# Performance work log

Measured on AMD Instinct MI355X. Metric: run time of the kernel, lower is better.

The kernel has to match this reference:

```python
import jax, jax.numpy as jnp
import numpy as np

B, S, V, E, D, C = 128, 256, 50000, 300, 200, 3

def setup_inputs() -> dict:
    key = jax.random.key(0)
    ks = jax.random.split(key, 16)
    std = 0.01  # truncated_normal(stddev=0.01) in the original
    d = {
        'x1': jax.random.randint(ks[0], (B, S), 0, V, dtype=jnp.int32),
        'x2': jax.random.randint(ks[1], (B, S), 0, V, dtype=jnp.int32),
        'len1': jax.random.randint(ks[2], (B,), 1, S + 1, dtype=jnp.int32),
        'len2': jax.random.randint(ks[3], (B,), 1, S + 1, dtype=jnp.int32),
        'emb': jax.random.normal(ks[4], (V, E), jnp.float32),
        'W_proj': jax.random.normal(ks[5], (E, D), jnp.float32) * std,
        'F_W1': jax.random.normal(ks[6], (D, D), jnp.float32) * std,
        'F_b1': jnp.zeros((D,), jnp.float32),
        'F_W2': jax.random.normal(ks[7], (D, D), jnp.float32) * std,
        'F_b2': jnp.zeros((D,), jnp.float32),
        'G_W1': jax.random.normal(ks[8], (2 * D, D), jnp.float32) * std,
        'G_b1': jnp.zeros((D,), jnp.float32),
        'G_W2': jax.random.normal(ks[9], (D, D), jnp.float32) * std,
        'G_b2': jnp.zeros((D,), jnp.float32),
        'H_W1': jax.random.normal(ks[10], (2 * D, D), jnp.float32) * std,
        'H_b1': jnp.zeros((D,), jnp.float32),
        'H_W2': jax.random.normal(ks[11], (D, D), jnp.float32) * std,
        'H_b2': jnp.zeros((D,), jnp.float32),
        'W_out': jax.random.normal(ks[12], (D, C), jnp.float32) * std,
        'b_out': jnp.zeros((C,), jnp.float32),
    }
    return d


def _mlp(x, W1, b1, W2, b2):
    # two dense layers, relu after each (activation_fn defaults to relu)
    h = jax.nn.relu(x @ W1 + b1)
    return jax.nn.relu(h @ W2 + b2)


def reference(x1, x2, len1, len2, emb, W_proj,
              F_W1, F_b1, F_W2, F_b2,
              G_W1, G_b1, G_W2, G_b2,
              H_W1, H_b1, H_W2, H_b2,
              W_out, b_out):
    seq = x1.shape[1]
    # masks: [B, S, 1]
    pos = jnp.arange(seq)
    mask1 = (pos[None, :] < len1[:, None]).astype(jnp.float32)[..., None]
    mask2 = (pos[None, :] < len2[:, None]).astype(jnp.float32)[..., None]

    # embed (L2-normalized table) + project to D
    emb_n = emb * jax.lax.rsqrt(jnp.sum(emb * emb, axis=1, keepdims=True))
    e1, e2 = emb_n[x1], emb_n[x2]          # [B,S,E]
    x1p, x2p = e1 @ W_proj, e2 @ W_proj    # [B,S,D]

    # attend: F(x1) . F(x2) -> [B,S1,S2] (broadcast-mul-reduce == contraction)
    f1 = _mlp(x1p, F_W1, F_b1, F_W2, F_b2)
    f2 = _mlp(x2p, F_W1, F_b1, F_W2, F_b2)
    sim = jnp.einsum('bid,bjd->bij', f1, f2)
    sim = sim * (mask1 * jnp.swapaxes(mask2, 1, 2))  # multiplicative mask (as in source)

    alpha = jnp.einsum('bji,bid->bjd', jax.nn.softmax(jnp.swapaxes(sim, 1, 2), axis=-1), x1p)  # [B,S2,D]
    beta = jnp.einsum('bij,bjd->bid', jax.nn.softmax(sim, axis=-1), x2p)                        # [B,S1,D]

    # compare
    v1 = _mlp(jnp.concatenate([x1p, beta], axis=2), G_W1, G_b1, G_W2, G_b2)
    v2 = _mlp(jnp.concatenate([x2p, alpha], axis=2), G_W1, G_b1, G_W2, G_b2)

    # aggregate
    v1 = jnp.sum(v1 * mask1, axis=1)  # [B,D]
    v2 = jnp.sum(v2 * mask2, axis=1)
    h = _mlp(jnp.concatenate([v1, v2], axis=1), H_W1, H_b1, H_W2, H_b2)
    y_hat = h @ W_out + b_out  # [B,C] logits
    return y_hat
```

## Files before the change

kernel.cpp:

```cpp
#include <hip/hip_runtime.h>
#include <math.h>

#define B_ 128
#define S_ 256
#define V_ 50000
#define E_ 300
#define D_ 200
#define C_ 3
#define P_ 256
#define TOK_ (B_*S_)

typedef __attribute__((ext_vector_type(8))) short bf16x8;
typedef __attribute__((ext_vector_type(4))) float f32x4;

static __device__ __forceinline__ short f2bf(float f) {
  unsigned u = __builtin_bit_cast(unsigned, f);
  u += 0x7fffu + ((u >> 16) & 1u);
  return (short)(u >> 16);
}
static __device__ __forceinline__ float bf2f(unsigned short u) {
  unsigned v = ((unsigned)u) << 16;
  return __builtin_bit_cast(float, v);
}

__global__ void pad2d_kernel(const float* __restrict__ src, float* __restrict__ dst,
                             int sR, int sC, int dR, int dC) {
  int idx = blockIdx.x * 256 + threadIdx.x;
  if (idx >= dR * dC) return;
  int r = idx / dC, c = idx - r * dC;
  dst[idx] = (r < sR && c < sC) ? src[r * sC + c] : 0.0f;
}

__global__ void padcat_kernel(const float* __restrict__ src, float* __restrict__ dst) {
  int idx = blockIdx.x * 256 + threadIdx.x;
  if (idx >= 512 * 256) return;
  int r = idx >> 8, c = idx & 255;
  int sr = (r < 200) ? r : ((r >= 256 && r < 456) ? (r - 56) : -1);
  dst[idx] = (sr >= 0 && c < 200) ? src[sr * 200 + c] : 0.0f;
}

__global__ void padT_bf16(const float* __restrict__ src, unsigned short* __restrict__ dst,
                          int sK, int sN, int dK, int dN) {
  int idx = blockIdx.x * 256 + threadIdx.x;
  if (idx >= dN * dK) return;
  int n = idx / dK, k = idx - n * dK;
  float v = (k < sK && n < sN) ? src[k * sN + n] : 0.0f;
  dst[idx] = (unsigned short)f2bf(v);
}

__global__ void padcatT_bf16(const float* __restrict__ src, unsigned short* __restrict__ dst) {
  int idx = blockIdx.x * 256 + threadIdx.x;
  if (idx >= 256 * 512) return;
  int n = idx >> 9, k = idx & 511;
  int sk = (k < 256) ? ((k < 200) ? k : -1) : (((k - 256) < 200) ? (200 + k - 256) : -1);
  float v = (sk >= 0 && n < 200) ? src[sk * 200 + n] : 0.0f;
  dst[idx] = (unsigned short)f2bf(v);
}

__global__ void zero_kernel(float* __restrict__ p, int n) {
  int idx = blockIdx.x * 256 + threadIdx.x;
  if (idx < n) p[idx] = 0.0f;
}

__global__ void concat_ids_kernel(const int* __restrict__ a, const int* __restrict__ b,
                                  int* __restrict__ dst) {
  int i = blockIdx.x * 256 + threadIdx.x;
  if (i < TOK_) dst[i] = a[i];
  else if (i < 2 * TOK_) dst[i] = b[i - TOK_];
}

__global__ void concat_lens_kernel(const int* __restrict__ a, const int* __restrict__ b,
                                   int* __restrict__ dst) {
  int i = threadIdx.x;
  if (i < B_) dst[i] = a[i];
  else dst[i] = b[i - B_];
}

__global__ __launch_bounds__(256) void invnorm_kernel(const int* __restrict__ ids,
    const float* __restrict__ emb, float* __restrict__ invn) {
  int tok = blockIdx.x * 4 + (threadIdx.x >> 6);
  int l = threadIdx.x & 63;
  long base = (long)ids[tok] * E_;
  float ss = 0.0f;
  for (int e = l; e < E_; e += 64) { float v = emb[base + e]; ss += v * v; }
  #pragma unroll
  for (int d = 32; d >= 1; d >>= 1) ss += __shfl_xor(ss, d, 64);
  if (l == 0) invn[tok] = 1.0f / sqrtf(ss);
}

__global__ __launch_bounds__(256) void transpose_bf16(
    const unsigned short* __restrict__ in, unsigned short* __restrict__ outp) {
  __shared__ unsigned short t[64][66];
  const int b = blockIdx.x;
  const int r0 = blockIdx.y * 64, c0 = blockIdx.z * 64;
  const unsigned short* src = in + (long)b * S_ * P_;
  unsigned short* dst = outp + (long)b * P_ * S_;
  const int tx = threadIdx.x & 63, ty = threadIdx.x >> 6;
  #pragma unroll
  for (int i = 0; i < 16; ++i)
    t[ty * 16 + i][tx] = src[(long)(r0 + ty * 16 + i) * P_ + c0 + tx];
  __syncthreads();
  #pragma unroll
  for (int i = 0; i < 16; ++i)
    dst[(long)(c0 + ty * 16 + i) * S_ + r0 + tx] = t[tx][ty * 16 + i];
}

template<int MODE, bool RELU, bool AGG>
__global__ __launch_bounds__(512) void gemm_mfma(
    const unsigned short* __restrict__ A1, const unsigned short* __restrict__ A2,
    const int* __restrict__ ids, const float* __restrict__ emb,
    const float* __restrict__ invn,
    const unsigned short* __restrict__ WT, const float* __restrict__ bias,
    unsigned short* __restrict__ outp, float* __restrict__ aggOut,
    const int* __restrict__ lens, int K)
{
  __shared__ unsigned short As[128 * 32];
  __shared__ unsigned short Bs[256 * 32];
  const int tid = threadIdx.x;
  const int lane = tid & 63;
  const int w = tid >> 6;
  const int wr = w >> 2, wc = w & 3;
  const long t0 = (long)blockIdx.x * 128;
  const int g = lane >> 4, ln = lane & 15;

  f32x4 acc[4][4];
  #pragma unroll
  for (int i = 0; i < 4; ++i)
    #pragma unroll
    for (int j = 0; j < 4; ++j) acc[i][j] = (f32x4){0.f, 0.f, 0.f, 0.f};

  const int arow = tid >> 2, aks = tid & 3;

  for (int k0 = 0; k0 < K; k0 += 32) {
    {
      bf16x8 v;
      if (MODE == 1) {
        const long t = t0 + arow;
        const long base = (long)ids[t] * E_;
        const float inv = invn[t];
        const int kb = k0 + aks * 8;
        short tmp[8];
        #pragma unroll
        for (int i = 0; i < 8; ++i) {
          const int k = kb + i;
          tmp[i] = f2bf((k < E_) ? emb[base + k] * inv : 0.0f);
        }
        #pragma unroll
        for (int i = 0; i < 8; ++i) v[i] = tmp[i];
      } else if (MODE == 2) {
        const unsigned short* src = (k0 < P_) ? (A1 + (t0 + arow) * P_ + k0)
                                              : (A2 + (t0 + arow) * P_ + (k0 - P_));
        v = *(const bf16x8*)(src + aks * 8);
      } else {
        v = *(const bf16x8*)(A1 + (t0 + arow) * P_ + k0 + aks * 8);
      }
      const int slot = aks ^ ((arow >> 1) & 3);
      *(bf16x8*)&As[arow * 32 + slot * 8] = v;
    }
    #pragma unroll
    for (int cc = 0; cc < 2; ++cc) {
      const int c = tid + cc * 512;
      const int col = c >> 2, ks = c & 3;
      bf16x8 v = *(const bf16x8*)(WT + (long)col * K + k0 + ks * 8);
      const int slot = ks ^ ((col >> 1) & 3);
      *(bf16x8*)&Bs[col * 32 + slot * 8] = v;
    }
    __syncthreads();
    bf16x8 af[4], bfr[4];
    #pragma unroll
    for (int fr = 0; fr < 4; ++fr) {
      const int row = wr * 64 + fr * 16 + ln;
      af[fr] = *(const bf16x8*)&As[row * 32 + ((g ^ ((row >> 1) & 3)) * 8)];
    }
    #pragma unroll
    for (int fc = 0; fc < 4; ++fc) {
      const int col = wc * 64 + fc * 16 + ln;
      bfr[fc] = *(const bf16x8*)&Bs[col * 32 + ((g ^ ((col >> 1) & 3)) * 8)];
    }
    #pragma unroll
    for (int fr = 0; fr < 4; ++fr)
      #pragma unroll
      for (int fc = 0; fc < 4; ++fc)
        acc[fr][fc] = __builtin_amdgcn_mfma_f32_16x16x32_bf16(af[fr], bfr[fc], acc[fr][fc], 0, 0, 0);
    __syncthreads();
  }

  const int g4 = g * 4;
  if (AGG) {
    const int b = (int)(t0 >> 8);
    const int s0 = (int)(t0 & 255);
    const int len = lens[b];
    #pragma unroll
    for (int fc = 0; fc < 4; ++fc) {
      const int col = wc * 64 + fc * 16 + ln;
      const float bb = bias[col];
      float sum = 0.0f;
      #pragma unroll
      for (int fr = 0; fr < 4; ++fr) {
        const int sbase = s0 + wr * 64 + fr * 16 + g4;
        #pragma unroll
        for (int r = 0; r < 4; ++r) {
          if (sbase + r < len) sum += fmaxf(acc[fr][fc][r] + bb, 0.0f);
        }
      }
      sum += __shfl_xor(sum, 16, 64);
      sum += __shfl_xor(sum, 32, 64);
      if (g == 0) atomicAdd(&aggOut[(long)b * P_ + col], sum);
    }
  } else {
    #pragma unroll
    for (int fc = 0; fc < 4; ++fc) {
      const int col = wc * 64 + fc * 16 + ln;
      const float bb = bias ? bias[col] : 0.0f;
      #pragma unroll
      for (int fr = 0; fr < 4; ++fr) {
        const long rbase = t0 + wr * 64 + fr * 16 + g4;
        #pragma unroll
        for (int r = 0; r < 4; ++r) {
          float v = acc[fr][fc][r] + bb;
          if (RELU) v = fmaxf(v, 0.0f);
          outp[(rbase + r) * P_ + col] = (unsigned short)f2bf(v);
        }
      }
    }
  }
}

__global__ __launch_bounds__(512) void attend_fused(
    const unsigned short* __restrict__ f12, const unsigned short* __restrict__ x12T,
    const int* __restrict__ lens12, unsigned short* __restrict__ out12)
{
  __shared__ unsigned short As[128 * 32];
  __shared__ unsigned short Bs[256 * 32];
  __shared__ unsigned short Pt[128 * 256];
  __shared__ float redmax[128][4];
  __shared__ float redsum[128][4];

  const int tid = threadIdx.x;
  const int lane = tid & 63;
  const int w = tid >> 6;
  const int wr = w >> 2, wc = w & 3;
  const int b = blockIdx.y;
  const int z = blockIdx.z;
  const int i0 = blockIdx.x * 128;
  const int g = lane >> 4, ln = lane & 15;

  const unsigned short* Afeat = f12 + (size_t)z * TOK_ * P_;
  const unsigned short* Bfeat = f12 + (size_t)(1 - z) * TOK_ * P_;
  const unsigned short* XT    = x12T + (size_t)(1 - z) * TOK_ * P_;
  unsigned short* outp        = out12 + (size_t)z * TOK_ * P_;
  const int l1 = lens12[z * B_ + b];
  const int l2 = lens12[(1 - z) * B_ + b];

  const unsigned short* Arows = Afeat + ((long)b * S_ + i0) * P_;
  const unsigned short* Brows = Bfeat + (long)b * S_ * P_;

  f32x4 acc[4][4];
  #pragma unroll
  for (int i = 0; i < 4; ++i)
    #pragma unroll
    for (int j = 0; j < 4; ++j) acc[i][j] = (f32x4){0.f, 0.f, 0.f, 0.f};

  const int arow = tid >> 2, aks = tid & 3;
  for (int k0 = 0; k0 < P_; k0 += 32) {
    {
      bf16x8 v = *(const bf16x8*)(Arows + (long)arow * P_ + k0 + aks * 8);
      const int slot = aks ^ ((arow >> 1) & 3);
      *(bf16x8*)&As[arow * 32 + slot * 8] = v;
    }
    #pragma unroll
    for (int cc = 0; cc < 2; ++cc) {
      const int c = tid + cc * 512;
      const int col = c >> 2, ks = c & 3;
      bf16x8 v = *(const bf16x8*)(Brows + (long)col * P_ + k0 + ks * 8);
      const int slot = ks ^ ((col >> 1) & 3);
      *(bf16x8*)&Bs[col * 32 + slot * 8] = v;
    }
    __syncthreads();
    bf16x8 af[4], bfr[4];
    #pragma unroll
    for (int fr = 0; fr < 4; ++fr) {
      const int row = wr * 64 + fr * 16 + ln;
      af[fr] = *(const bf16x8*)&As[row * 32 + ((g ^ ((row >> 1) & 3)) * 8)];
    }
    #pragma unroll
    for (int fc = 0; fc < 4; ++fc) {
      const int col = wc * 64 + fc * 16 + ln;
      bfr[fc] = *(const bf16x8*)&Bs[col * 32 + ((g ^ ((col >> 1) & 3)) * 8)];
    }
    #pragma unroll
    for (int fr = 0; fr < 4; ++fr)
      #pragma unroll
      for (int fc = 0; fc < 4; ++fc)
        acc[fr][fc] = __builtin_amdgcn_mfma_f32_16x16x32_bf16(af[fr], bfr[fc], acc[fr][fc], 0, 0, 0);
    __syncthreads();
  }

  const int g4 = g * 4;
  #pragma unroll
  for (int fr = 0; fr < 4; ++fr) {
    #pragma unroll
    for (int fc = 0; fc < 4; ++fc) {
      const int col = wc * 64 + fc * 16 + ln;
      const float mj = (col < l2) ? 1.0f : 0.0f;
      #pragma unroll
      for (int r = 0; r < 4; ++r) {
        const int rowg = i0 + wr * 64 + fr * 16 + g4 + r;
        acc[fr][fc][r] *= (rowg < l1) ? mj : 0.0f;
      }
    }
  }
  #pragma unroll
  for (int fr = 0; fr < 4; ++fr) {
    #pragma unroll
    for (int r = 0; r < 4; ++r) {
      float m = fmaxf(fmaxf(acc[fr][0][r], acc[fr][1][r]),
                      fmaxf(acc[fr][2][r], acc[fr][3][r]));
      m = fmaxf(m, __shfl_xor(m, 1, 64));
      m = fmaxf(m, __shfl_xor(m, 2, 64));
      m = fmaxf(m, __shfl_xor(m, 4, 64));
      m = fmaxf(m, __shfl_xor(m, 8, 64));
      if (ln == 0) redmax[wr * 64 + fr * 16 + g4 + r][wc] = m;
    }
  }
  __syncthreads();
  #pragma unroll
  for (int fr = 0; fr < 4; ++fr) {
    #pragma unroll
    for (int r = 0; r < 4; ++r) {
      const int lr = wr * 64 + fr * 16 + g4 + r;
      const float4 m4 = *(const float4*)redmax[lr];
      const float m = fmaxf(fmaxf(m4.x, m4.y), fmaxf(m4.z, m4.w));
      float s = 0.0f;
      #pragma unroll
      for (int fc = 0; fc < 4; ++fc) {
        const float e = __expf(acc[fr][fc][r] - m);
        acc[fr][fc][r] = e;
        s += e;
      }
      s += __shfl_xor(s, 1, 64);
      s += __shfl_xor(s, 2, 64);
      s += __shfl_xor(s, 4, 64);
      s += __shfl_xor(s, 8, 64);
      if (ln == 0) redsum[lr][wc] = s;
    }
  }
  __syncthreads();
  #pragma unroll
  for (int fr = 0; fr < 4; ++fr) {
    #pragma unroll
    for (int r = 0; r < 4; ++r) {
      const int lr = wr * 64 + fr * 16 + g4 + r;
      const float4 s4 = *(const float4*)redsum[lr];
      const float inv = 1.0f / (s4.x + s4.y + s4.z + s4.w);
      #pragma unroll
      for (int fc = 0; fc < 4; ++fc) {
        const int col = wc * 64 + fc * 16 + ln;
        Pt[lr * 256 + ((col & ~31) | ((((col >> 3) & 3) ^ ((lr >> 1) & 3)) << 3) | (col & 7))] =
            (unsigned short)f2bf(acc[fr][fc][r] * inv);
      }
    }
  }

  f32x4 acc2[4][4];
  #pragma unroll
  for (int i = 0; i < 4; ++i)
    #pragma unroll
    for (int j = 0; j < 4; ++j) acc2[i][j] = (f32x4){0.f, 0.f, 0.f, 0.f};
  const unsigned short* XTb = XT + (long)b * P_ * S_;
  for (int k0 = 0; k0 < S_; k0 += 32) {
    #pragma unroll
    for (int cc = 0; cc < 2; ++cc) {
      const int c = tid + cc * 512;
      const int col = c >> 2, ks = c & 3;
      bf16x8 v = *(const bf16x8*)(XTb + (long)col * S_ + k0 + ks * 8);
      const int slot = ks ^ ((col >> 1) & 3);
      *(bf16x8*)&Bs[col * 32 + slot * 8] = v;
    }
    __syncthreads();
    bf16x8 af[4], bfr[4];
    #pragma unroll
    for (int fr = 0; fr < 4; ++fr) {
      const int row = wr * 64 + fr * 16 + ln;
      af[fr] = *(const bf16x8*)&Pt[row * 256 + k0 + ((g ^ ((row >> 1) & 3)) * 8)];
    }
    #pragma unroll
    for (int fc = 0; fc < 4; ++fc) {
      const int col = wc * 64 + fc * 16 + ln;
      bfr[fc] = *(const bf16x8*)&Bs[col * 32 + ((g ^ ((col >> 1) & 3)) * 8)];
    }
    #pragma unroll
    for (int fr = 0; fr < 4; ++fr)
      #pragma unroll
      for (int fc = 0; fc < 4; ++fc)
        acc2[fr][fc] = __builtin_amdgcn_mfma_f32_16x16x32_bf16(af[fr], bfr[fc], acc2[fr][fc], 0, 0, 0);
    __syncthreads();
  }

  #pragma unroll
  for (int fc = 0; fc < 4; ++fc) {
    const int col = wc * 64 + fc * 16 + ln;
    #pragma unroll
    for (int fr = 0; fr < 4; ++fr) {
      const long rbase = (long)b * S_ + i0 + wr * 64 + fr * 16 + g4;
      #pragma unroll
      for (int r = 0; r < 4; ++r)
        outp[(rbase + r) * P_ + col] = (unsigned short)f2bf(acc2[fr][fc][r]);
    }
  }
}

__global__ __launch_bounds__(256) void head_kernel(
    const float* __restrict__ v1s, const float* __restrict__ v2s,
    const float* __restrict__ HW1p, const float* __restrict__ Hb1p,
    const float* __restrict__ HW2p, const float* __restrict__ Hb2p,
    const float* __restrict__ Wout, const float* __restrict__ bout,
    float* __restrict__ y)
{
  __shared__ float xin[2 * P_];
  __shared__ float h[P_];
  const int b = blockIdx.x;
  const int tid = threadIdx.x;
  xin[tid] = v1s[(long)b * P_ + tid];
  xin[P_ + tid] = v2s[(long)b * P_ + tid];
  __syncthreads();
  float acc = Hb1p[tid];
  for (int e = 0; e < 2 * P_; ++e) acc += xin[e] * HW1p[(long)e * P_ + tid];
  h[tid] = fmaxf(acc, 0.0f);
  __syncthreads();
  float acc2 = Hb2p[tid];
  for (int e = 0; e < P_; ++e) acc2 += h[e] * HW2p[(long)e * P_ + tid];
  const float h2 = fmaxf(acc2, 0.0f);
  __syncthreads();
  xin[tid] = h2;
  __syncthreads();
  if (tid < C_) {
    float a = bout[tid];
    for (int d = 0; d < D_; ++d) a += xin[d] * Wout[d * C_ + tid];
    y[(long)b * C_ + tid] = a;
  }
}

extern "C" void kernel_launch(void* const* d_in, const int* in_sizes, int n_in,
                              void* d_out, int out_size, void* d_ws, size_t ws_size,
                              hipStream_t stream)
{
  const int*   x1    = (const int*)d_in[0];
  const int*   x2    = (const int*)d_in[1];
  const int*   len1  = (const int*)d_in[2];
  const int*   len2  = (const int*)d_in[3];
  const float* emb   = (const float*)d_in[4];
  const float* Wproj = (const float*)d_in[5];
  const float* FW1   = (const float*)d_in[6];
  const float* Fb1   = (const float*)d_in[7];
  const float* FW2   = (const float*)d_in[8];
  const float* Fb2   = (const float*)d_in[9];
  const float* GW1   = (const float*)d_in[10];
  const float* Gb1   = (const float*)d_in[11];
  const float* GW2   = (const float*)d_in[12];
  const float* Gb2   = (const float*)d_in[13];
  const float* HW1   = (const float*)d_in[14];
  const float* Hb1   = (const float*)d_in[15];
  const float* HW2   = (const float*)d_in[16];
  const float* Hb2   = (const float*)d_in[17];
  const float* Wout  = (const float*)d_in[18];
  const float* bout  = (const float*)d_in[19];
  float* out = (float*)d_out;

  float* ws = (float*)d_ws;
  size_t o = 0;
  auto alloc = [&](size_t n) { float* p = ws + o; o += n; return p; };
  float* v12   = alloc((size_t)2 * B_ * P_);
  float* invn12 = alloc((size_t)2 * TOK_);
  float* HW1p  = alloc((size_t)2 * P_ * P_); float* Hb1p = alloc(P_);
  float* HW2p  = alloc((size_t)P_ * P_);     float* Hb2p = alloc(P_);
  float* Fb1p  = alloc(P_); float* Fb2p = alloc(P_);
  float* Gb1p  = alloc(P_); float* Gb2p = alloc(P_);
  int* ids12  = (int*)alloc((size_t)2 * TOK_);
  int* lens12 = (int*)alloc(2 * B_);
  unsigned short* us = (unsigned short*)(ws + o);
  size_t uo = 0;
  auto ualloc = [&](size_t n) { unsigned short* p = us + uo; uo += n; return p; };
  unsigned short* x12b  = ualloc((size_t)2 * TOK_ * P_);
  unsigned short* hid2b = ualloc((size_t)2 * TOK_ * P_);
  unsigned short* f12b  = ualloc((size_t)2 * TOK_ * P_);
  unsigned short* ba12b = ualloc((size_t)2 * TOK_ * P_);
  unsigned short* x12T  = ualloc((size_t)2 * TOK_ * P_);
  unsigned short* WpT   = ualloc((size_t)P_ * 320);
  unsigned short* FW1T  = ualloc((size_t)P_ * P_);
  unsigned short* FW2T  = ualloc((size_t)P_ * P_);
  unsigned short* GW1T  = ualloc((size_t)P_ * 2 * P_);
  unsigned short* GW2T  = ualloc((size_t)P_ * P_);
  if (o * sizeof(float) + uo * sizeof(unsigned short) > ws_size) return;

  float* v1s = v12;
  float* v2s = v12 + (size_t)B_ * P_;

  auto g = [](int n) { return (n + 255) / 256; };

  padT_bf16<<<g(P_ * 320), 256, 0, stream>>>(Wproj, WpT, E_, D_, 320, P_);
  padT_bf16<<<g(P_ * P_), 256, 0, stream>>>(FW1, FW1T, D_, D_, P_, P_);
  padT_bf16<<<g(P_ * P_), 256, 0, stream>>>(FW2, FW2T, D_, D_, P_, P_);
  padT_bf16<<<g(P_ * P_), 256, 0, stream>>>(GW2, GW2T, D_, D_, P_, P_);
  padcatT_bf16<<<g(P_ * 2 * P_), 256, 0, stream>>>(GW1, GW1T);
  padcat_kernel<<<g(2 * P_ * P_), 256, 0, stream>>>(HW1, HW1p);
  pad2d_kernel<<<g(P_ * P_), 256, 0, stream>>>(HW2, HW2p, D_, D_, P_, P_);
  pad2d_kernel<<<1, 256, 0, stream>>>(Fb1, Fb1p, 1, D_, 1, P_);
  pad2d_kernel<<<1, 256, 0, stream>>>(Fb2, Fb2p, 1, D_, 1, P_);
  pad2d_kernel<<<1, 256, 0, stream>>>(Gb1, Gb1p, 1, D_, 1, P_);
  pad2d_kernel<<<1, 256, 0, stream>>>(Gb2, Gb2p, 1, D_, 1, P_);
  pad2d_kernel<<<1, 256, 0, stream>>>(Hb1, Hb1p, 1, D_, 1, P_);
  pad2d_kernel<<<1, 256, 0, stream>>>(Hb2, Hb2p, 1, D_, 1, P_);
  zero_kernel<<<g(2 * B_ * P_), 256, 0, stream>>>(v12, 2 * B_ * P_);
  concat_ids_kernel<<<g(2 * TOK_), 256, 0, stream>>>(x1, x2, ids12);
  concat_lens_kernel<<<1, 256, 0, stream>>>(len1, len2, lens12);

  invnorm_kernel<<<2 * TOK_ / 4, 256, 0, stream>>>(ids12, emb, invn12);
  gemm_mfma<1, false, false><<<2 * TOK_ / 128, 512, 0, stream>>>(
      nullptr, nullptr, ids12, emb, invn12, WpT, nullptr, x12b, nullptr, nullptr, 320);

  {
    dim3 grid(2 * B_, 4, 4);
    transpose_bf16<<<grid, 256, 0, stream>>>(x12b, x12T);
  }

  gemm_mfma<0, true, false><<<2 * TOK_ / 128, 512, 0, stream>>>(
      x12b, nullptr, nullptr, nullptr, nullptr, FW1T, Fb1p, hid2b, nullptr, nullptr, P_);
  gemm_mfma<0, true, false><<<2 * TOK_ / 128, 512, 0, stream>>>(
      hid2b, nullptr, nullptr, nullptr, nullptr, FW2T, Fb2p, f12b, nullptr, nullptr, P_);

  {
    dim3 grid(S_ / 128, B_, 2);
    attend_fused<<<grid, 512, 0, stream>>>(f12b, x12T, lens12, ba12b);
  }

  gemm_mfma<2, true, false><<<2 * TOK_ / 128, 512, 0, stream>>>(
      x12b, ba12b, nullptr, nullptr, nullptr, GW1T, Gb1p, hid2b, nullptr, nullptr, 2 * P_);
  gemm_mfma<0, true, true><<<2 * TOK_ / 128, 512, 0, stream>>>(
      hid2b, nullptr, nullptr, nullptr, nullptr, GW2T, Gb2p, nullptr, v12, lens12, P_);

  head_kernel<<<B_, 256, 0, stream>>>(v1s, v2s, HW1p, Hb1p, HW2p, Hb2p, Wout, bout, out);
}
```

Baseline: 411.7 us.

## Fuse MLP layer pairs, merge prep kernels, widen blocks to 1024 threads

Merges the sixteen small padding, transpose, zero and concat kernels into one prep_all launch. Fuses each two-layer MLP (F and G) into one kernel that keeps the hidden activation in LDS, so the bf16 intermediate never goes to global memory. The fused MLP and attend kernels now use 1024 threads with 16 waves, each wave holding a 64x32 tile. The cost is 64KB+ of LDS per block and 16 waves per workgroup, which lowers occupancy and adds sync overhead.

```diff
diff --git a/kernel.cpp b/kernel.cpp
--- a/kernel.cpp
+++ b/kernel.cpp
@@ -18,62 +18,69 @@
   u += 0x7fffu + ((u >> 16) & 1u);
   return (short)(u >> 16);
 }
-static __device__ __forceinline__ float bf2f(unsigned short u) {
-  unsigned v = ((unsigned)u) << 16;
-  return __builtin_bit_cast(float, v);
-}
-
-__global__ void pad2d_kernel(const float* __restrict__ src, float* __restrict__ dst,
-                             int sR, int sC, int dR, int dC) {
-  int idx = blockIdx.x * 256 + threadIdx.x;
-  if (idx >= dR * dC) return;
-  int r = idx / dC, c = idx - r * dC;
-  dst[idx] = (r < sR && c < sC) ? src[r * sC + c] : 0.0f;
-}
-
-__global__ void padcat_kernel(const float* __restrict__ src, float* __restrict__ dst) {
-  int idx = blockIdx.x * 256 + threadIdx.x;
-  if (idx >= 512 * 256) return;
-  int r = idx >> 8, c = idx & 255;
-  int sr = (r < 200) ? r : ((r >= 256 && r < 456) ? (r - 56) : -1);
-  dst[idx] = (sr >= 0 && c < 200) ? src[sr * 200 + c] : 0.0f;
-}
-
-__global__ void padT_bf16(const float* __restrict__ src, unsigned short* __restrict__ dst,
-                          int sK, int sN, int dK, int dN) {
-  int idx = blockIdx.x * 256 + threadIdx.x;
-  if (idx >= dN * dK) return;
-  int n = idx / dK, k = idx - n * dK;
-  float v = (k < sK && n < sN) ? src[k * sN + n] : 0.0f;
-  dst[idx] = (unsigned short)f2bf(v);
-}
-
-__global__ void padcatT_bf16(const float* __restrict__ src, unsigned short* __restrict__ dst) {
-  int idx = blockIdx.x * 256 + threadIdx.x;
-  if (idx >= 256 * 512) return;
-  int n = idx >> 9, k = idx & 511;
-  int sk = (k < 256) ? ((k < 200) ? k : -1) : (((k - 256) < 200) ? (200 + k - 256) : -1);
-  float v = (sk >= 0 && n < 200) ? src[sk * 200 + n] : 0.0f;
-  dst[idx] = (unsigned short)f2bf(v);
-}
-
-__global__ void zero_kernel(float* __restrict__ p, int n) {
-  int idx = blockIdx.x * 256 + threadIdx.x;
-  if (idx < n) p[idx] = 0.0f;
-}
-
-__global__ void concat_ids_kernel(const int* __restrict__ a, const int* __restrict__ b,
-                                  int* __restrict__ dst) {
-  int i = blockIdx.x * 256 + threadIdx.x;
-  if (i < TOK_) dst[i] = a[i];
-  else if (i < 2 * TOK_) dst[i] = b[i - TOK_];
-}
-
-__global__ void concat_lens_kernel(const int* __restrict__ a, const int* __restrict__ b,
-                                   int* __restrict__ dst) {
-  int i = threadIdx.x;
-  if (i < B_) dst[i] = a[i];
-  else dst[i] = b[i - B_];
+
+__global__ __launch_bounds__(256) void prep_all(
+    const float* __restrict__ Wproj, const float* __restrict__ FW1,
+    const float* __restrict__ FW2, const float* __restrict__ GW1,
+    const float* __restrict__ GW2, const float* __restrict__ HW1,
+    const float* __restrict__ HW2,
+    const float* __restrict__ Fb1, const float* __restrict__ Fb2,
+    const float* __restrict__ Gb1, const float* __restrict__ Gb2,
+    const float* __restrict__ Hb1, const float* __restrict__ Hb2,
+    const int* __restrict__ x1, const int* __restrict__ x2,
+    const int* __restrict__ len1, const int* __restrict__ len2,
+    unsigned short* __restrict__ WpT, unsigned short* __restrict__ FW1T,
+    unsigned short* __restrict__ FW2T, unsigned short* __restrict__ GW1T,
+    unsigned short* __restrict__ GW2T, float* __restrict__ HW1p,
+    float* __restrict__ HW2p, float* __restrict__ biases,
+    float* __restrict__ v12, int* __restrict__ ids12, int* __restrict__ lens12)
+{
+  const int blk = blockIdx.x;
+  const int tid = threadIdx.x;
+  if (blk < 320) {
+    int idx = blk * 256 + tid;
+    int n = idx / 320, k = idx - n * 320;
+    WpT[idx] = (unsigned short)f2bf((k < E_ && n < D_) ? Wproj[k * D_ + n] : 0.0f);
+  } else if (blk < 576) {
+    int idx = (blk - 320) * 256 + tid;
+    int n = idx >> 8, k = idx & 255;
+    FW1T[idx] = (unsigned short)f2bf((k < D_ && n < D_) ? FW1[k * D_ + n] : 0.0f);
+  } else if (blk < 832) {
+    int idx = (blk - 576) * 256 + tid;
+    int n = idx >> 8, k = idx & 255;
+    FW2T[idx] = (unsigned short)f2bf((k < D_ && n < D_) ? FW2[k * D_ + n] : 0.0f);
+  } else if (blk < 1088) {
+    int idx = (blk - 832) * 256 + tid;
+    int n = idx >> 8, k = idx & 255;
+    GW2T[idx] = (unsigned short)f2bf((k < D_ && n < D_) ? GW2[k * D_ + n] : 0.0f);
+  } else if (blk < 1600) {
+    int idx = (blk - 1088) * 256 + tid;
+    int n = idx >> 9, k = idx & 511;
+    int sk = (k < 256) ? ((k < D_) ? k : -1) : (((k - 256) < D_) ? (D_ + k - 256) : -1);
+    GW1T[idx] = (unsigned short)f2bf((sk >= 0 && n < D_) ? GW1[sk * D_ + n] : 0.0f);
+  } else if (blk < 2112) {
+    int idx = (blk - 1600) * 256 + tid;
+    int r = idx >> 8, c = idx & 255;
+    int sr = (r < D_) ? r : ((r >= 256 && r < 256 + D_) ? (r - 56) : -1);
+    HW1p[idx] = (sr >= 0 && c < D_) ? HW1[sr * D_ + c] : 0.0f;
+  } else if (blk < 2368) {
+    int idx = (blk - 2112) * 256 + tid;
+    int r = idx >> 8, c = idx & 255;
+    HW2p[idx] = (r < D_ && c < D_) ? HW2[r * D_ + c] : 0.0f;
+  } else if (blk < 2374) {
+    int j = blk - 2368;
+    const float* src = (j == 0) ? Fb1 : (j == 1) ? Fb2 : (j == 2) ? Gb1
+                      : (j == 3) ? Gb2 : (j == 4) ? Hb1 : Hb2;
+    biases[j * 256 + tid] = (tid < D_) ? src[tid] : 0.0f;
+  } else if (blk < 2630) {
+    v12[(blk - 2374) * 256 + tid] = 0.0f;
+  } else if (blk < 2886) {
+    int idx = (blk - 2630) * 256 + tid;
+    ids12[idx] = (idx < TOK_) ? x1[idx] : x2[idx - TOK_];
+  } else {
+    if (tid < B_) lens12[tid] = len1[tid];
+    else if (tid < 2 * B_) lens12[tid] = len2[tid - B_];
+  }
 }
 
 __global__ __launch_bounds__(256) void invnorm_kernel(const int* __restrict__ ids,
@@ -105,14 +112,10 @@
     dst[(long)(c0 + ty * 16 + i) * S_ + r0 + tx] = t[tx][ty * 16 + i];
 }
 
-template<int MODE, bool RELU, bool AGG>
-__global__ __launch_bounds__(512) void gemm_mfma(
-    const unsigned short* __restrict__ A1, const unsigned short* __restrict__ A2,
+__global__ __launch_bounds__(512) void proj_mfma(
     const int* __restrict__ ids, const float* __restrict__ emb,
-    const float* __restrict__ invn,
-    const unsigned short* __restrict__ WT, const float* __restrict__ bias,
-    unsigned short* __restrict__ outp, float* __restrict__ aggOut,
-    const int* __restrict__ lens, int K)
+    const float* __restrict__ invn, const unsigned short* __restrict__ WT,
+    unsigned short* __restrict__ outp, int K)
 {
   __shared__ unsigned short As[128 * 32];
   __shared__ unsigned short Bs[256 * 32];
@@ -130,30 +133,21 @@
     for (int j = 0; j < 4; ++j) acc[i][j] = (f32x4){0.f, 0.f, 0.f, 0.f};
 
   const int arow = tid >> 2, aks = tid & 3;
-
   for (int k0 = 0; k0 < K; k0 += 32) {
     {
+      const long t = t0 + arow;
+      const long base = (long)ids[t] * E_;
+      const float inv = invn[t];
+      const int kb = k0 + aks * 8;
+      short tmp[8];
+      #pragma unroll
+      for (int i = 0; i < 8; ++i) {
+        const int k = kb + i;
+        tmp[i] = f2bf((k < E_) ? emb[base + k] * inv : 0.0f);
+      }
       bf16x8 v;
-      if (MODE == 1) {
-        const long t = t0 + arow;
-        const long base = (long)ids[t] * E_;
-        const float inv = invn[t];
-        const int kb = k0 + aks * 8;
-        short tmp[8];
-        #pragma unroll
-        for (int i = 0; i < 8; ++i) {
-          const int k = kb + i;
-          tmp[i] = f2bf((k < E_) ? emb[base + k] * inv : 0.0f);
-        }
-        #pragma unroll
-        for (int i = 0; i < 8; ++i) v[i] = tmp[i];
-      } else if (MODE == 2) {
-        const unsigned short* src = (k0 < P_) ? (A1 + (t0 + arow) * P_ + k0)
-                                              : (A2 + (t0 + arow) * P_ + (k0 - P_));
-        v = *(const bf16x8*)(src + aks * 8);
-      } else {
-        v = *(const bf16x8*)(A1 + (t0 + arow) * P_ + k0 + aks * 8);
-      }
+      #pragma unroll
+      for (int i = 0; i < 8; ++i) v[i] = tmp[i];
       const int slot = aks ^ ((arow >> 1) & 3);
       *(bf16x8*)&As[arow * 32 + slot * 8] = v;
     }
@@ -184,23 +178,149 @@
         acc[fr][fc] = __builtin_amdgcn_mfma_f32_16x16x32_bf16(af[fr], bfr[fc], acc[fr][fc], 0, 0, 0);
     __syncthreads();
   }
-
   const int g4 = g * 4;
+  #pragma unroll
+  for (int fc = 0; fc < 4; ++fc) {
+    const int col = wc * 64 + fc * 16 + ln;
+    #pragma unroll
+    for (int fr = 0; fr < 4; ++fr) {
+      const long rbase = t0 + wr * 64 + fr * 16 + g4;
+      #pragma unroll
+      for (int r = 0; r < 4; ++r)
+        outp[(rbase + r) * P_ + col] = (unsigned short)f2bf(acc[fr][fc][r]);
+    }
+  }
+}
+
+template<int MODE1, bool AGG>
+__global__ __launch_bounds__(1024) void fused_mlp(
+    const unsigned short* __restrict__ A1, const unsigned short* __restrict__ A2,
+    const unsigned short* __restrict__ W1T, const float* __restrict__ b1,
+    const unsigned short* __restrict__ W2T, const float* __restrict__ b2,
+    unsigned short* __restrict__ outp, float* __restrict__ aggOut,
+    const int* __restrict__ lens, int K1)
+{
+  __shared__ unsigned short As[128 * 32];
+  __shared__ unsigned short Bs[256 * 32];
+  __shared__ unsigned short Hs[128 * 256];
+  const int tid = threadIdx.x;
+  const int lane = tid & 63;
+  const int w = tid >> 6;
+  const int wr = w >> 3, wc = w & 7;
+  const long t0 = (long)blockIdx.x * 128;
+  const int g = lane >> 4, ln = lane & 15;
+  const int g4 = g * 4;
+
+  f32x4 acc[4][2];
+  #pragma unroll
+  for (int i = 0; i < 4; ++i)
+    #pragma unroll
+    for (int j = 0; j < 2; ++j) acc[i][j] = (f32x4){0.f, 0.f, 0.f, 0.f};
+
+  for (int k0 = 0; k0 < K1; k0 += 32) {
+    if (tid < 512) {
+      const int arow = tid >> 2, aks = tid & 3;
+      bf16x8 v;
+      if (MODE1 == 2) {
+        const unsigned short* src = (k0 < P_) ? (A1 + (t0 + arow) * P_ + k0)
+                                              : (A2 + (t0 + arow) * P_ + (k0 - P_));
+        v = *(const bf16x8*)(src + aks * 8);
+      } else {
+        v = *(const bf16x8*)(A1 + (t0 + arow) * P_ + k0 + aks * 8);
+      }
+      const int slot = aks ^ ((arow >> 1) & 3);
+      *(bf16x8*)&As[arow * 32 + slot * 8] = v;
+    }
+    {
+      const int col = tid >> 2, ks = tid & 3;
+      bf16x8 v = *(const bf16x8*)(W1T + (long)col * K1 + k0 + ks * 8);
+      const int slot = ks ^ ((col >> 1) & 3);
+      *(bf16x8*)&Bs[col * 32 + slot * 8] = v;
+    }
+    __syncthreads();
+    bf16x8 af[4], bfr[2];
+    #pragma unroll
+    for (int fr = 0; fr < 4; ++fr) {
+      const int row = wr * 64 + fr * 16 + ln;
+      af[fr] = *(const bf16x8*)&As[row * 32 + ((g ^ ((row >> 1) & 3)) * 8)];
+    }
+    #pragma unroll
+    for (int fc = 0; fc < 2; ++fc) {
+      const int col = wc * 32 + fc * 16 + ln;
+      bfr[fc] = *(const bf16x8*)&Bs[col * 32 + ((g ^ ((col >> 1) & 3)) * 8)];
+    }
+    #pragma unroll
+    for (int fr = 0; fr < 4; ++fr)
+      #pragma unroll
+      for (int fc = 0; fc < 2; ++fc)
+        acc[fr][fc] = __builtin_amdgcn_mfma_f32_16x16x32_bf16(af[fr], bfr[fc], acc[fr][fc], 0, 0, 0);
+    __syncthreads();
+  }
+
+  #pragma unroll
+  for (int fc = 0; fc < 2; ++fc) {
+    const int col = wc * 32 + fc * 16 + ln;
+    const float bb = b1[col];
+    #pragma unroll
+    for (int fr = 0; fr < 4; ++fr) {
+      #pragma unroll
+      for (int r = 0; r < 4; ++r) {
+        const int lr = wr * 64 + fr * 16 + g4 + r;
+        const float v = fmaxf(acc[fr][fc][r] + bb, 0.0f);
+        Hs[lr * 256 + ((col & ~31) | ((((col >> 3) & 3) ^ ((lr >> 1) & 3)) << 3) | (col & 7))] =
+            (unsigned short)f2bf(v);
+      }
+    }
+  }
+
+  f32x4 acc2[4][2];
+  #pragma unroll
+  for (int i = 0; i < 4; ++i)
+    #pragma unroll
+    for (int j = 0; j < 2; ++j) acc2[i][j] = (f32x4){0.f, 0.f, 0.f, 0.f};
+
+  for (int k0 = 0; k0 < 256; k0 += 32) {
+    {
+      const int col = tid >> 2, ks = tid & 3;
+      bf16x8 v = *(const bf16x8*)(W2T + (long)col * 256 + k0 + ks * 8);
+      const int slot = ks ^ ((col >> 1) & 3);
+      *(bf16x8*)&Bs[col * 32 + slot * 8] = v;
+    }
+    __syncthreads();
+    bf16x8 af[4], bfr[2];
+    #pragma unroll
+    for (int fr = 0; fr < 4; ++fr) {
+      const int row = wr * 64 + fr * 16 + ln;
+      af[fr] = *(const bf16x8*)&Hs[row * 256 + k0 + ((g ^ ((row >> 1) & 3)) * 8)];
+    }
+    #pragma unroll
+    for (int fc = 0; fc < 2; ++fc) {
+      const int col = wc * 32 + fc * 16 + ln;
+      bfr[fc] = *(const bf16x8*)&Bs[col * 32 + ((g ^ ((col >> 1) & 3)) * 8)];
+    }
+    #pragma unroll
+    for (int fr = 0; fr < 4; ++fr)
+      #pragma unroll
+      for (int fc = 0; fc < 2; ++fc)
+        acc2[fr][fc] = __builtin_amdgcn_mfma_f32_16x16x32_bf16(af[fr], bfr[fc], acc2[fr][fc], 0, 0, 0);
+    __syncthreads();
+  }
+
   if (AGG) {
     const int b = (int)(t0 >> 8);
     const int s0 = (int)(t0 & 255);
     const int len = lens[b];
     #pragma unroll
-    for (int fc = 0; fc < 4; ++fc) {
-      const int col = wc * 64 + fc * 16 + ln;
-      const float bb = bias[col];
+    for (int fc = 0; fc < 2; ++fc) {
+      const int col = wc * 32 + fc * 16 + ln;
+      const float bb = b2[col];
       float sum = 0.0f;
       #pragma unroll
       for (int fr = 0; fr < 4; ++fr) {
         const int sbase = s0 + wr * 64 + fr * 16 + g4;
         #pragma unroll
         for (int r = 0; r < 4; ++r) {
-          if (sbase + r < len) sum += fmaxf(acc[fr][fc][r] + bb, 0.0f);
+          if (sbase + r < len) sum += fmaxf(acc2[fr][fc][r] + bb, 0.0f);
         }
       }
       sum += __shfl_xor(sum, 16, 64);
@@ -209,41 +329,39 @@
     }
   } else {
     #pragma unroll
-    for (int fc = 0; fc < 4; ++fc) {
-      const int col = wc * 64 + fc * 16 + ln;
-      const float bb = bias ? bias[col] : 0.0f;
+    for (int fc = 0; fc < 2; ++fc) {
+      const int col = wc * 32 + fc * 16 + ln;
+      const float bb = b2[col];
       #pragma unroll
       for (int fr = 0; fr < 4; ++fr) {
         const long rbase = t0 + wr * 64 + fr * 16 + g4;
         #pragma unroll
-        for (int r = 0; r < 4; ++r) {
-          float v = acc[fr][fc][r] + bb;
-          if (RELU) v = fmaxf(v, 0.0f);
-          outp[(rbase + r) * P_ + col] = (unsigned short)f2bf(v);
-        }
-      }
-    }
-  }
-}
-
-__global__ __launch_bounds__(512) void attend_fused(
+        for (int r = 0; r < 4; ++r)
+          outp[(rbase + r) * P_ + col] = (unsigned short)f2bf(fmaxf(acc2[fr][fc][r] + bb, 0.0f));
+      }
+    }
+  }
+}
+
+__global__ __launch_bounds__(1024) void attend_fused(
     const unsigned short* __restrict__ f12, const unsigned short* __restrict__ x12T,
     const int* __restrict__ lens12, unsigned short* __restrict__ out12)
 {
   __shared__ unsigned short As[128 * 32];
   __shared__ unsigned short Bs[256 * 32];
   __shared__ unsigned short Pt[128 * 256];
-  __shared__ float redmax[128][4];
-  __shared__ float redsum[128][4];
+  __shared__ float redmax[128][8];
+  __shared__ float redsum[128][8];
 
   const int tid = threadIdx.x;
   const int lane = tid & 63;
   const int w = tid >> 6;
-  const int wr = w >> 2, wc = w & 3;
+  const int wr = w >> 3, wc = w & 7;
   const int b = blockIdx.y;
   const int z = blockIdx.z;
   const int i0 = blockIdx.x * 128;
   const int g = lane >> 4, ln = lane & 15;
+  const int g4 = g * 4;
 
   const unsigned short* Afeat = f12 + (size_t)z * TOK_ * P_;
   const unsigned short* Bfeat = f12 + (size_t)(1 - z) * TOK_ * P_;
@@ -255,54 +373,51 @@
   const unsigned short* Arows = Afeat + ((long)b * S_ + i0) * P_;
   const unsigned short* Brows = Bfeat + (long)b * S_ * P_;
 
-  f32x4 acc[4][4];
+  f32x4 acc[4][2];
   #pragma unroll
   for (int i = 0; i < 4; ++i)
     #pragma unroll
-    for (int j = 0; j < 4; ++j) acc[i][j] = (f32x4){0.f, 0.f, 0.f, 0.f};
-
-  const int arow = tid >> 2, aks = tid & 3;
+    for (int j = 0; j < 2; ++j) acc[i][j] = (f32x4){0.f, 0.f, 0.f, 0.f};
+
   for (int k0 = 0; k0 < P_; k0 += 32) {
-    {
+    if (tid < 512) {
+      const int arow = tid >> 2, aks = tid & 3;
       bf16x8 v = *(const bf16x8*)(Arows + (long)arow * P_ + k0 + aks * 8);
       const int slot = aks ^ ((arow >> 1) & 3);
       *(bf16x8*)&As[arow * 32 + slot * 8] = v;
     }
-    #pragma unroll
-    for (int cc = 0; cc < 2; ++cc) {
-      const int c = tid + cc * 512;
-      const int col = c >> 2, ks = c & 3;
+    {
+      const int col = tid >> 2, ks = tid & 3;
       bf16x8 v = *(const bf16x8*)(Brows + (long)col * P_ + k0 + ks * 8);
       const int slot = ks ^ ((col >> 1) & 3);
       *(bf16x8*)&Bs[col * 32 + slot * 8] = v;
     }
     __syncthreads();
-    bf16x8 af[4], bfr[4];
+    bf16x8 af[4], bfr[2];
     #pragma unroll
     for (int fr = 0; fr < 4; ++fr) {
       const int row = wr * 64 + fr * 16 + ln;
       af[fr] = *(const bf16x8*)&As[row * 32 + ((g ^ ((row >> 1) & 3)) * 8)];
     }
     #pragma unroll
-    for (int fc = 0; fc < 4; ++fc) {
-      const int col = wc * 64 + fc * 16 + ln;
+    for (int fc = 0; fc < 2; ++fc) {
+      const int col = wc * 32 + fc * 16 + ln;
       bfr[fc] = *(const bf16x8*)&Bs[col * 32 + ((g ^ ((col >> 1) & 3)) * 8)];
     }
     #pragma unroll
     for (int fr = 0; fr < 4; ++fr)
       #pragma unroll
-      for (int fc = 0; fc < 4; ++fc)
+      for (int fc = 0; fc < 2; ++fc)
         acc[fr][fc] = __builtin_amdgcn_mfma_f32_16x16x32_bf16(af[fr], bfr[fc], acc[fr][fc], 0, 0, 0);
     __syncthreads();
   }
 
-  const int g4 = g * 4;
-  #pragma unroll
-  for (int fr = 0; fr < 4; ++fr) {
-    #pragma unroll
-    for (int fc = 0; fc < 4; ++fc) {
-      const int col = wc * 64 + fc * 16 + ln;
-      const float mj = (col < l2) ? 1.0f : 0.0f;
+  #pragma unroll
+  for (int fc = 0; fc < 2; ++fc) {
+    const int col = wc * 32 + fc * 16 + ln;
+    const float mj = (col < l2) ? 1.0f : 0.0f;
+    #pragma unroll
+    for (int fr = 0; fr < 4; ++fr) {
       #pragma unroll
       for (int r = 0; r < 4; ++r) {
         const int rowg = i0 + wr * 64 + fr * 16 + g4 + r;
@@ -314,8 +429,7 @@
   for (int fr = 0; fr < 4; ++fr) {
     #pragma unroll
     for (int r = 0; r < 4; ++r) {
-      float m = fmaxf(fmaxf(acc[fr][0][r], acc[fr][1][r]),
-                      fmaxf(acc[fr][2][r], acc[fr][3][r]));
+      float m = fmaxf(acc[fr][0][r], acc[fr][1][r]);
       m = fmaxf(m, __shfl_xor(m, 1, 64));
       m = fmaxf(m, __shfl_xor(m, 2, 64));
       m = fmaxf(m, __shfl_xor(m, 4, 64));
@@ -329,11 +443,13 @@
     #pragma unroll
     for (int r = 0; r < 4; ++r) {
       const int lr = wr * 64 + fr * 16 + g4 + r;
-      const float4 m4 = *(const float4*)redmax[lr];
-      const float m = fmaxf(fmaxf(m4.x, m4.y), fmaxf(m4.z, m4.w));
+      const float4 a4 = *(const float4*)&redmax[lr][0];
+      const float4 b4 = *(const float4*)&redmax[lr][4];
+      const float m = fmaxf(fmaxf(fmaxf(a4.x, a4.y), fmaxf(a4.z, a4.w)),
+                            fmaxf(fmaxf(b4.x, b4.y), fmaxf(b4.z, b4.w)));
       float s = 0.0f;
       #pragma unroll
-      for (int fc = 0; fc < 4; ++fc) {
+      for (int fc = 0; fc < 2; ++fc) {
         const float e = __expf(acc[fr][fc][r] - m);
         acc[fr][fc][r] = e;
         s += e;
@@ -351,55 +467,54 @@
     #pragma unroll
     for (int r = 0; r < 4; ++r) {
       const int lr = wr * 64 + fr * 16 + g4 + r;
-      const float4 s4 = *(const float4*)redsum[lr];
-      const float inv = 1.0f / (s4.x + s4.y + s4.z + s4.w);
-      #pragma unroll
-      for (int fc = 0; fc < 4; ++fc) {
-        const int col = wc * 64 + fc * 16 + ln;
+      const float4 a4 = *(const float4*)&redsum[lr][0];
+      const float4 b4 = *(const float4*)&redsum[lr][4];
+      const float inv = 1.0f / (a4.x + a4.y + a4.z + a4.w + b4.x + b4.y + b4.z + b4.w);
+      #pragma unroll
+      for (int fc = 0; fc < 2; ++fc) {
+        const int col = wc * 32 + fc * 16 + ln;
         Pt[lr * 256 + ((col & ~31) | ((((col >> 3) & 3) ^ ((lr >> 1) & 3)) << 3) | (col & 7))] =
             (unsigned short)f2bf(acc[fr][fc][r] * inv);
       }
     }
   }
 
-  f32x4 acc2[4][4];
+  f32x4 acc2[4][2];
   #pragma unroll
   for (int i = 0; i < 4; ++i)
     #pragma unroll
-    for (int j = 0; j < 4; ++j) acc2[i][j] = (f32x4){0.f, 0.f, 0.f, 0.f};
+    for (int j = 0; j < 2; ++j) acc2[i][j] = (f32x4){0.f, 0.f, 0.f, 0.f};
   const unsigned short* XTb = XT + (long)b * P_ * S_;
   for (int k0 = 0; k0 < S_; k0 += 32) {
-    #pragma unroll
-    for (int cc = 0; cc < 2; ++cc) {
-      const int c = tid + cc * 512;
-      const int col = c >> 2, ks = c & 3;
+    {
+      const int col = tid >> 2, ks = tid & 3;
       bf16x8 v = *(const bf16x8*)(XTb + (long)col * S_ + k0 + ks * 8);
       const int slot = ks ^ ((col >> 1) & 3);
       *(bf16x8*)&Bs[col * 32 + slot * 8] = v;
     }
     __syncthreads();
-    bf16x8 af[4], bfr[4];
+    bf16x8 af[4], bfr[2];
     #pragma unroll
     for (int fr = 0; fr < 4; ++fr) {
       const int row = wr * 64 + fr * 16 + ln;
       af[fr] = *(const bf16x8*)&Pt[row * 256 + k0 + ((g ^ ((row >> 1) & 3)) * 8)];
     }
     #pragma unroll
-    for (int fc = 0; fc < 4; ++fc) {
-      const int col = wc * 64 + fc * 16 + ln;
+    for (int fc = 0; fc < 2; ++fc) {
+      const int col = wc * 32 + fc * 16 + ln;
       bfr[fc] = *(const bf16x8*)&Bs[col * 32 + ((g ^ ((col >> 1) & 3)) * 8)];
     }
     #pragma unroll
     for (int fr = 0; fr < 4; ++fr)
       #pragma unroll
-      for (int fc = 0; fc < 4; ++fc)
+      for (int fc = 0; fc < 2; ++fc)
         acc2[fr][fc] = __builtin_amdgcn_mfma_f32_16x16x32_bf16(af[fr], bfr[fc], acc2[fr][fc], 0, 0, 0);
     __syncthreads();
   }
 
   #pragma unroll
-  for (int fc = 0; fc < 4; ++fc) {
-    const int col = wc * 64 + fc * 16 + ln;
+  for (int fc = 0; fc < 2; ++fc) {
+    const int col = wc * 32 + fc * 16 + ln;
     #pragma unroll
     for (int fr = 0; fr < 4; ++fr) {
       const long rbase = (long)b * S_ + i0 + wr * 64 + fr * 16 + g4;
@@ -470,19 +585,17 @@
   float* ws = (float*)d_ws;
   size_t o = 0;
   auto alloc = [&](size_t n) { float* p = ws + o; o += n; return p; };
-  float* v12   = alloc((size_t)2 * B_ * P_);
+  float* v12    = alloc((size_t)2 * B_ * P_);
   float* invn12 = alloc((size_t)2 * TOK_);
-  float* HW1p  = alloc((size_t)2 * P_ * P_); float* Hb1p = alloc(P_);
-  float* HW2p  = alloc((size_t)P_ * P_);     float* Hb2p = alloc(P_);
-  float* Fb1p  = alloc(P_); float* Fb2p = alloc(P_);
-  float* Gb1p  = alloc(P_); float* Gb2p = alloc(P_);
+  float* HW1p   = alloc((size_t)2 * P_ * P_);
+  float* HW2p   = alloc((size_t)P_ * P_);
+  float* biases = alloc((size_t)6 * 256);
   int* ids12  = (int*)alloc((size_t)2 * TOK_);
   int* lens12 = (int*)alloc(2 * B_);
   unsigned short* us = (unsigned short*)(ws + o);
   size_t uo = 0;
   auto ualloc = [&](size_t n) { unsigned short* p = us + uo; uo += n; return p; };
   unsigned short* x12b  = ualloc((size_t)2 * TOK_ * P_);
-  unsigned short* hid2b = ualloc((size_t)2 * TOK_ * P_);
   unsigned short* f12b  = ualloc((size_t)2 * TOK_ * P_);
   unsigned short* ba12b = ualloc((size_t)2 * TOK_ * P_);
   unsigned short* x12T  = ualloc((size_t)2 * TOK_ * P_);
@@ -493,51 +606,40 @@
   unsigned short* GW2T  = ualloc((size_t)P_ * P_);
   if (o * sizeof(float) + uo * sizeof(unsigned short) > ws_size) return;
 
+  float* Fb1p = biases + 0;
+  float* Fb2p = biases + 256;
+  float* Gb1p = biases + 512;
+  float* Gb2p = biases + 768;
+  float* Hb1p = biases + 1024;
+  float* Hb2p = biases + 1280;
   float* v1s = v12;
   float* v2s = v12 + (size_t)B_ * P_;
 
-  auto g = [](int n) { return (n + 255) / 256; };
-
-  padT_bf16<<<g(P_ * 320), 256, 0, stream>>>(Wproj, WpT, E_, D_, 320, P_);
-  padT_bf16<<<g(P_ * P_), 256, 0, stream>>>(FW1, FW1T, D_, D_, P_, P_);
-  padT_bf16<<<g(P_ * P_), 256, 0, stream>>>(FW2, FW2T, D_, D_, P_, P_);
-  padT_bf16<<<g(P_ * P_), 256, 0, stream>>>(GW2, GW2T, D_, D_, P_, P_);
-  padcatT_bf16<<<g(P_ * 2 * P_), 256, 0, stream>>>(GW1, GW1T);
-  padcat_kernel<<<g(2 * P_ * P_), 256, 0, stream>>>(HW1, HW1p);
-  pad2d_kernel<<<g(P_ * P_), 256, 0, stream>>>(HW2, HW2p, D_, D_, P_, P_);
-  pad2d_kernel<<<1, 256, 0, stream>>>(Fb1, Fb1p, 1, D_, 1, P_);
-  pad2d_kernel<<<1, 256, 0, stream>>>(Fb2, Fb2p, 1, D_, 1, P_);
-  pad2d_kernel<<<1, 256, 0, stream>>>(Gb1, Gb1p, 1, D_, 1, P_);
-  pad2d_kernel<<<1, 256, 0, stream>>>(Gb2, Gb2p, 1, D_, 1, P_);
-  pad2d_kernel<<<1, 256, 0, stream>>>(Hb1, Hb1p, 1, D_, 1, P_);
-  pad2d_kernel<<<1, 256, 0, stream>>>(Hb2, Hb2p, 1, D_, 1, P_);
-  zero_kernel<<<g(2 * B_ * P_), 256, 0, stream>>>(v12, 2 * B_ * P_);
-  concat_ids_kernel<<<g(2 * TOK_), 256, 0, stream>>>(x1, x2, ids12);
-  concat_lens_kernel<<<1, 256, 0, stream>>>(len1, len2, lens12);
+  prep_all<<<2887, 256, 0, stream>>>(
+      Wproj, FW1, FW2, GW1, GW2, HW1, HW2,
+      Fb1, Fb2, Gb1, Gb2, Hb1, Hb2,
+      x1, x2, len1, len2,
+      WpT, FW1T, FW2T, GW1T, GW2T, HW1p, HW2p, biases, v12, ids12, lens12);
 
   invnorm_kernel<<<2 * TOK_ / 4, 256, 0, stream>>>(ids12, emb, invn12);
-  gemm_mfma<1, false, false><<<2 * TOK_ / 128, 512, 0, stream>>>(
-      nullptr, nullptr, ids12, emb, invn12, WpT, nullptr, x12b, nullptr, nullptr, 320);
+
+  proj_mfma<<<2 * TOK_ / 128, 512, 0, stream>>>(ids12, emb, invn12, WpT, x12b, 320);
 
   {
     dim3 grid(2 * B_, 4, 4);
     transpose_bf16<<<grid, 256, 0, stream>>>(x12b, x12T);
   }
 
-  gemm_mfma<0, true, false><<<2 * TOK_ / 128, 512, 0, stream>>>(
-      x12b, nullptr, nullptr, nullptr, nullptr, FW1T, Fb1p, hid2b, nullptr, nullptr, P_);
-  gemm_mfma<0, true, false><<<2 * TOK_ / 128, 512, 0, stream>>>(
-      hid2b, nullptr, nullptr, nullptr, nullptr, FW2T, Fb2p, f12b, nullptr, nullptr, P_);
+  fused_mlp<0, false><<<2 * TOK_ / 128, 1024, 0, stream>>>(
+      x12b, nullptr, FW1T, Fb1p, FW2T, Fb2p, f12b, nullptr, nullptr, P_);
 
   {
     dim3 grid(S_ / 128, B_, 2);
-    attend_fused<<<grid, 512, 0, stream>>>(f12b, x12T, lens12, ba12b);
-  }
-
-  gemm_mfma<2, true, false><<<2 * TOK_ / 128, 512, 0, stream>>>(
-      x12b, ba12b, nullptr, nullptr, nullptr, GW1T, Gb1p, hid2b, nullptr, nullptr, 2 * P_);
-  gemm_mfma<0, true, true><<<2 * TOK_ / 128, 512, 0, stream>>>(
-      hid2b, nullptr, nullptr, nullptr, nullptr, GW2T, Gb2p, nullptr, v12, lens12, P_);
+    attend_fused<<<grid, 1024, 0, stream>>>(f12b, x12T, lens12, ba12b);
+  }
+
+  fused_mlp<2, true><<<2 * TOK_ / 128, 1024, 0, stream>>>(
+      x12b, ba12b, GW1T, Gb1p, GW2T, Gb2p, nullptr, v12, lens12, 2 * P_);
 
   head_kernel<<<B_, 256, 0, stream>>>(v1s, v2s, HW1p, Hb1p, HW2p, Hb2p, Wout, bout, out);
 }
```

Result: faster. 397.6 us (-3.4%).
